# Kernel optimization log

Measured on AMD Instinct MI355X. Metric: run time of the kernel, lower is better.

The kernel has to match this reference:

```python
import jax, jax.numpy as jnp
import numpy as np

DIM = 512
NUM_HEADS = 8
HEAD_DIM = DIM // NUM_HEADS
SCALE = HEAD_DIM ** -0.5


def setup_inputs() -> dict:
    key = jax.random.key(0)
    ks = jax.random.split(key, 6)
    B, N, C = 2, 4096, DIM
    s = C ** -0.5  # init scale, torch Linear default-ish
    return {
        "x": jax.random.normal(ks[0], (B, N, C), dtype=jnp.float32),
        "Wq": jax.random.normal(ks[1], (C, C), dtype=jnp.float32) * s,
        "Wk": jax.random.normal(ks[2], (C, C), dtype=jnp.float32) * s,
        "Wv": jax.random.normal(ks[3], (C, C), dtype=jnp.float32) * s,
        "Wo": jax.random.normal(ks[4], (C, C), dtype=jnp.float32) * s,
        "bo": jax.random.normal(ks[5], (C,), dtype=jnp.float32) * s,
    }


def reference(x, Wq, Wk, Wv, Wo, bo):
    B, N, C = x.shape
    H, D = NUM_HEADS, HEAD_DIM
    # torch nn.Linear: y = x @ W.T
    q = (x @ Wq.T).reshape(B, N, H, D).transpose(0, 2, 1, 3)  # [B,H,N,D]
    k = (x @ Wk.T).reshape(B, N, H, D).transpose(0, 2, 1, 3)
    v = (x @ Wv.T).reshape(B, N, H, D).transpose(0, 2, 1, 3)
    attn = jnp.einsum("bhnd,bhmd->bhnm", q, k) * SCALE  # [B,H,N,N]
    attn = jax.nn.softmax(attn, axis=-1)
    out = jnp.einsum("bhnm,bhmd->bhnd", attn, v)
    out = out.transpose(0, 2, 1, 3).reshape(B, N, C)
    return out @ Wo.T + bo
```

## Files before the change

kernel.cpp:

```cpp
#include <hip/hip_runtime.h>
#include <hip/hip_bf16.h>
#include <cstdint>
#include <cstddef>

using bf16 = __bf16;
typedef __attribute__((ext_vector_type(8))) __bf16 bf16x8;
typedef __attribute__((ext_vector_type(4))) float  f32x4;

#define LOG2E 1.4426950408889634f

__device__ inline void gld_lds16(const void* g, void* l) {
  __builtin_amdgcn_global_load_lds(
      (const __attribute__((address_space(1))) void*)g,
      (__attribute__((address_space(3))) void*)l, 16, 0, 0);
}

__global__ __launch_bounds__(256) void k_cvt(const float* __restrict__ s,
                                             bf16* __restrict__ d, int n8) {
  int i = blockIdx.x * 256 + threadIdx.x;
  if (i >= n8) return;
  const float4* p = ((const float4*)s) + (size_t)i * 2;
  float4 a = p[0], b = p[1];
  bf16x8 o;
  o[0] = (bf16)a.x; o[1] = (bf16)a.y; o[2] = (bf16)a.z; o[3] = (bf16)a.w;
  o[4] = (bf16)b.x; o[5] = (bf16)b.y; o[6] = (bf16)b.z; o[7] = (bf16)b.w;
  *(bf16x8*)(d + (size_t)i * 8) = o;
}

__global__ __launch_bounds__(256) void k_cvtw(
    const float* __restrict__ wq, const float* __restrict__ wk,
    const float* __restrict__ wv, const float* __restrict__ wo,
    bf16* __restrict__ wqkv, bf16* __restrict__ wob) {
  int i = blockIdx.x * 256 + threadIdx.x;
  int which = i >> 15, local = i & 32767;
  const float* s = (which == 0) ? wq : (which == 1) ? wk : (which == 2) ? wv : wo;
  bf16* d = (which < 3) ? (wqkv + ((size_t)which << 18)) : wob;
  const float4* p = ((const float4*)s) + (size_t)local * 2;
  float4 a = p[0], b = p[1];
  bf16x8 o;
  o[0] = (bf16)a.x; o[1] = (bf16)a.y; o[2] = (bf16)a.z; o[3] = (bf16)a.w;
  o[4] = (bf16)b.x; o[5] = (bf16)b.y; o[6] = (bf16)b.z; o[7] = (bf16)b.w;
  *(bf16x8*)(d + (size_t)local * 8) = o;
}

__global__ __launch_bounds__(256) void k_gemm(
    const bf16* __restrict__ A, const bf16* __restrict__ B, int mode,
    bf16* __restrict__ Qb, bf16* __restrict__ Kb, bf16* __restrict__ Vtb,
    float* __restrict__ outf, const float* __restrict__ bias) {
  const int K = 512;
  __shared__ alignas(16) bf16 As[128 * 64];
  __shared__ alignas(16) bf16 Bs[64 * 64];
  const int tid = threadIdx.x;
  const int wave = tid >> 6, lane = tid & 63;
  const int l15 = lane & 15, l4 = lane >> 4;
  const int m0 = blockIdx.x * 128, n0 = blockIdx.y * 64;
  const int wr = wave >> 1, wc = wave & 1;
  f32x4 acc[4][2] = {};

  for (int k0 = 0; k0 < K; k0 += 64) {
#pragma unroll
    for (int it = 0; it < 4; ++it) {
      int c = it * 256 + tid;
      int row = c >> 3, kc = c & 7;
      int sb = (kc * 16) ^ ((row & 7) << 4);
      gld_lds16((const char*)A + ((size_t)(m0 + row) * K + k0) * 2 + sb,
                (char*)As + c * 16);
    }
#pragma unroll
    for (int it = 0; it < 2; ++it) {
      int c = it * 256 + tid;
      int row = c >> 3, kc = c & 7;
      int sb = (kc * 16) ^ ((row & 7) << 4);
      gld_lds16((const char*)B + ((size_t)(n0 + row) * K + k0) * 2 + sb,
                (char*)Bs + c * 16);
    }
    __syncthreads();
#pragma unroll
    for (int ks = 0; ks < 2; ++ks) {
      bf16x8 af[4], bff[2];
#pragma unroll
      for (int mf = 0; mf < 4; ++mf) {
        int r = wr * 64 + mf * 16 + l15;
        af[mf] = *(const bf16x8*)((const char*)As + r * 128 +
                                  ((ks * 64 + l4 * 16) ^ ((r & 7) << 4)));
      }
#pragma unroll
      for (int nf = 0; nf < 2; ++nf) {
        int r = wc * 32 + nf * 16 + l15;
        bff[nf] = *(const bf16x8*)((const char*)Bs + r * 128 +
                                   ((ks * 64 + l4 * 16) ^ ((r & 7) << 4)));
      }
#pragma unroll
      for (int mf = 0; mf < 4; ++mf)
#pragma unroll
        for (int nf = 0; nf < 2; ++nf)
          acc[mf][nf] = __builtin_amdgcn_mfma_f32_16x16x32_bf16(
              af[mf], bff[nf], acc[mf][nf], 0, 0, 0);
    }
    __syncthreads();
  }

#pragma unroll
  for (int mf = 0; mf < 4; ++mf)
#pragma unroll
    for (int nf = 0; nf < 2; ++nf)
#pragma unroll
      for (int r = 0; r < 4; ++r) {
        int m = m0 + wr * 64 + mf * 16 + l4 * 4 + r;
        int n = n0 + wc * 32 + nf * 16 + l15;
        float v = acc[mf][nf][r];
        if (mode == 1) {
          outf[(size_t)m * 512 + n] = v + bias[n];
        } else {
          int which = n >> 9, o = n & 511, h = o >> 6, d = o & 63;
          int b = m >> 12, nr = m & 4095;
          if (which == 0)
            Qb[((size_t)(b * 8 + h) * 4096 + nr) * 64 + d] = (bf16)(v * 0.125f);
          else if (which == 1)
            Kb[((size_t)(b * 8 + h) * 4096 + nr) * 64 + d] = (bf16)v;
          else
            Vtb[((size_t)((b * 8 + h) * 64 + d)) * 4096 + nr] = (bf16)v;
        }
      }
}

template <int SPLIT>
__global__ __launch_bounds__(256, 4) void k_attn_t(
    const bf16* __restrict__ Q, const bf16* __restrict__ Kg,
    const bf16* __restrict__ Vt, bf16* __restrict__ AO,
    float* __restrict__ pO, float* __restrict__ pD) {
  __shared__ alignas(16) bf16 Ks[64 * 64];
  __shared__ alignas(16) bf16 Vs[64 * 64];
  __shared__ alignas(16) bf16 Ps[4][16 * 64];
  const int tid = threadIdx.x, wave = tid >> 6, lane = tid & 63;
  const int l15 = lane & 15, l4 = lane >> 4;
  const int bh = blockIdx.y, q0 = blockIdx.x * 64;
  const int z = SPLIT ? blockIdx.z : 0;
  const int n_lo = SPLIT ? z * 2048 : 0;
  const int NT = SPLIT ? 32 : 64;
  const char* Qb = (const char*)(Q + (size_t)bh * 4096 * 64);
  const char* Kb = (const char*)(Kg + (size_t)bh * 4096 * 64);
  const char* Vb = (const char*)(Vt + (size_t)bh * 64 * 4096);

  const int c0 = tid, c1 = 256 + tid;
  const int row0 = c0 >> 3, sb0 = ((c0 & 7) * 16) ^ ((row0 & 7) << 4);
  const int row1 = c1 >> 3, sb1 = ((c1 & 7) * 16) ^ ((row1 & 7) << 4);
  const char* ksrc0 = Kb + (size_t)(n_lo + row0) * 128 + sb0;
  const char* ksrc1 = Kb + (size_t)(n_lo + row1) * 128 + sb1;
  const char* vsrc0 = Vb + (size_t)row0 * 8192 + (size_t)n_lo * 2 + sb0;
  const char* vsrc1 = Vb + (size_t)row1 * 8192 + (size_t)n_lo * 2 + sb1;
  char* kdst0 = (char*)Ks + c0 * 16;
  char* kdst1 = (char*)Ks + c1 * 16;
  char* vdst0 = (char*)Vs + c0 * 16;
  char* vdst1 = (char*)Vs + c1 * 16;

  const char* kf_p[2][4];
#pragma unroll
  for (int cf = 0; cf < 4; ++cf) {
    int kv = cf * 16 + l15;
#pragma unroll
    for (int ds = 0; ds < 2; ++ds)
      kf_p[ds][cf] = (const char*)Ks + kv * 128 +
                     ((ds * 64 + l4 * 16) ^ ((kv & 7) << 4));
  }
  const char* vf_p[4][2];
#pragma unroll
  for (int df = 0; df < 4; ++df) {
    int d = df * 16 + l15;
#pragma unroll
    for (int ks = 0; ks < 2; ++ks)
      vf_p[df][ks] = (const char*)Vs + d * 128 +
                     ((ks * 64 + l4 * 16) ^ ((d & 7) << 4));
  }
  char* pw_p[4][4];
#pragma unroll
  for (int r = 0; r < 4; ++r) {
    int q = l4 * 4 + r;
#pragma unroll
    for (int cf = 0; cf < 4; ++cf)
      pw_p[r][cf] = (char*)Ps[wave] + q * 128 +
                    (((cf * 16 + l15) * 2) ^ ((q & 7) << 4));
  }
  const char* pf_p[2];
#pragma unroll
  for (int ks = 0; ks < 2; ++ks)
    pf_p[ks] = (const char*)Ps[wave] + l15 * 128 +
               ((ks * 64 + l4 * 16) ^ ((l15 & 7) << 4));

  bf16x8 qf[2];
#pragma unroll
  for (int ds = 0; ds < 2; ++ds)
    qf[ds] = *(const bf16x8*)(Qb +
        ((size_t)(q0 + wave * 16 + l15) * 64 + ds * 32 + l4 * 8) * 2);

  bf16x8 vone;
#pragma unroll
  for (int j = 0; j < 8; ++j) vone[j] = (bf16)1.0f;

  f32x4 oacc[4] = {};
  f32x4 dacc = {};

  for (int t = 0; t < NT; ++t) {
    gld_lds16(ksrc0, kdst0);
    gld_lds16(vsrc0, vdst0);
    gld_lds16(ksrc1, kdst1);
    gld_lds16(vsrc1, vdst1);
    ksrc0 += 8192; ksrc1 += 8192;
    vsrc0 += 128;  vsrc1 += 128;
    __syncthreads();

    f32x4 s[4];
#pragma unroll
    for (int cf = 0; cf < 4; ++cf) {
      f32x4 z2 = {};
      z2 = __builtin_amdgcn_mfma_f32_16x16x32_bf16(
          qf[0], *(const bf16x8*)kf_p[0][cf], z2, 0, 0, 0);
      z2 = __builtin_amdgcn_mfma_f32_16x16x32_bf16(
          qf[1], *(const bf16x8*)kf_p[1][cf], z2, 0, 0, 0);
      s[cf] = z2;
    }

#pragma unroll
    for (int r = 0; r < 4; ++r)
#pragma unroll
      for (int cf = 0; cf < 4; ++cf) {
        float p = __builtin_amdgcn_exp2f(s[cf][r] * LOG2E);
        *(bf16*)pw_p[r][cf] = (bf16)p;
      }

    bf16x8 pf0 = *(const bf16x8*)pf_p[0];
    bf16x8 pf1 = *(const bf16x8*)pf_p[1];

    dacc = __builtin_amdgcn_mfma_f32_16x16x32_bf16(pf0, vone, dacc, 0, 0, 0);
    dacc = __builtin_amdgcn_mfma_f32_16x16x32_bf16(pf1, vone, dacc, 0, 0, 0);

#pragma unroll
    for (int df = 0; df < 4; ++df) {
      oacc[df] = __builtin_amdgcn_mfma_f32_16x16x32_bf16(
          pf0, *(const bf16x8*)vf_p[df][0], oacc[df], 0, 0, 0);
      oacc[df] = __builtin_amdgcn_mfma_f32_16x16x32_bf16(
          pf1, *(const bf16x8*)vf_p[df][1], oacc[df], 0, 0, 0);
    }
    __syncthreads();
  }

  if (SPLIT) {
    float* po = pO + (((size_t)(z * 16 + bh)) * 4096) * 64;
    float* pd = pD + ((size_t)(z * 16 + bh)) * 4096;
#pragma unroll
    for (int r = 0; r < 4; ++r) {
      int n = q0 + wave * 16 + l4 * 4 + r;
#pragma unroll
      for (int df = 0; df < 4; ++df)
        po[(size_t)n * 64 + df * 16 + l15] = oacc[df][r];
      if (l15 == 0) pd[n] = dacc[r];
    }
  } else {
    int b = bh >> 3, h = bh & 7;
#pragma unroll
    for (int r = 0; r < 4; ++r) {
      float inv = 1.0f / dacc[r];
      int n = q0 + wave * 16 + l4 * 4 + r;
#pragma unroll
      for (int df = 0; df < 4; ++df) {
        int d = df * 16 + l15;
        AO[((size_t)(b * 4096 + n)) * 512 + h * 64 + d] =
            (bf16)(oacc[df][r] * inv);
      }
    }
  }
}

__global__ __launch_bounds__(256) void k_comb(
    const float* __restrict__ pO, const float* __restrict__ pD,
    bf16* __restrict__ AO) {
  const size_t SO = (size_t)16 * 4096 * 64;
  const size_t SD = (size_t)16 * 4096;
  int i = blockIdx.x * 256 + threadIdx.x;
  int g = i >> 3, j = i & 7;
  float den = pD[g] + pD[g + SD];
  float inv = 1.0f / den;
  const float* a = pO + (size_t)g * 64 + j * 8;
  const float* b2 = a + SO;
  bf16x8 o;
#pragma unroll
  for (int t = 0; t < 8; ++t) o[t] = (bf16)((a[t] + b2[t]) * inv);
  int bh = g >> 12, n = g & 4095, b = bh >> 3, h = bh & 7;
  *(bf16x8*)(AO + ((size_t)(b * 4096 + n)) * 512 + h * 64 + j * 8) = o;
}

extern "C" void kernel_launch(void* const* d_in, const int* in_sizes, int n_in,
                              void* d_out, int out_size, void* d_ws,
                              size_t ws_size, hipStream_t stream) {
  const float* x  = (const float*)d_in[0];
  const float* Wq = (const float*)d_in[1];
  const float* Wk = (const float*)d_in[2];
  const float* Wv = (const float*)d_in[3];
  const float* Wo = (const float*)d_in[4];
  const float* bo = (const float*)d_in[5];
  float* out = (float*)d_out;

  char* ws = (char*)d_ws;
  bf16* xb   = (bf16*)(ws);
  bf16* wqkv = (bf16*)(ws + (8u << 20));
  bf16* wob  = (bf16*)(ws + (8u << 20) + 1572864u);
  bf16* Qb   = (bf16*)(ws + (10u << 20));
  bf16* Kb   = (bf16*)(ws + (18u << 20));
  bf16* Vtb  = (bf16*)(ws + (26u << 20));
  bf16* AOb  = (bf16*)(ws + (34u << 20));
  float* pD  = (float*)(ws + (42u << 20));
  float* pO  = (float*)(ws + (43u << 20));

  k_cvt<<<2048, 256, 0, stream>>>(x, xb, 524288);
  k_cvtw<<<512, 256, 0, stream>>>(Wq, Wk, Wv, Wo, wqkv, wob);

  k_gemm<<<dim3(64, 24), 256, 0, stream>>>(xb, wqkv, 0, Qb, Kb, Vtb,
                                           nullptr, nullptr);

  if (ws_size >= ((size_t)75 << 20)) {
    k_attn_t<1><<<dim3(64, 16, 2), 256, 0, stream>>>(Qb, Kb, Vtb, nullptr,
                                                     pO, pD);
    k_comb<<<2048, 256, 0, stream>>>(pO, pD, AOb);
  } else {
    k_attn_t<0><<<dim3(64, 16), 256, 0, stream>>>(Qb, Kb, Vtb, AOb,
                                                  nullptr, nullptr);
  }

  k_gemm<<<dim3(64, 8), 256, 0, stream>>>(AOb, wob, 1, nullptr, nullptr,
                                          nullptr, out, bo);
}
```

Measured before the change: 183.1 us.

## Process two 16-row query tiles per wave to reuse K/V fragments

```diff
diff --git a/kernel.cpp b/kernel.cpp
--- a/kernel.cpp
+++ b/kernel.cpp
@@ -131,10 +131,10 @@
     float* __restrict__ pO, float* __restrict__ pD) {
   __shared__ alignas(16) bf16 Ks[64 * 64];
   __shared__ alignas(16) bf16 Vs[64 * 64];
-  __shared__ alignas(16) bf16 Ps[4][16 * 64];
+  __shared__ alignas(16) bf16 Ps[4][32 * 64];
   const int tid = threadIdx.x, wave = tid >> 6, lane = tid & 63;
   const int l15 = lane & 15, l4 = lane >> 4;
-  const int bh = blockIdx.y, q0 = blockIdx.x * 64;
+  const int bh = blockIdx.y, q0 = blockIdx.x * 128;
   const int z = SPLIT ? blockIdx.z : 0;
   const int n_lo = SPLIT ? z * 2048 : 0;
   const int NT = SPLIT ? 32 : 64;
@@ -187,18 +187,20 @@
     pf_p[ks] = (const char*)Ps[wave] + l15 * 128 +
                ((ks * 64 + l4 * 16) ^ ((l15 & 7) << 4));
 
-  bf16x8 qf[2];
-#pragma unroll
-  for (int ds = 0; ds < 2; ++ds)
-    qf[ds] = *(const bf16x8*)(Qb +
-        ((size_t)(q0 + wave * 16 + l15) * 64 + ds * 32 + l4 * 8) * 2);
+  bf16x8 qf[2][2];
+#pragma unroll
+  for (int mrow = 0; mrow < 2; ++mrow)
+#pragma unroll
+    for (int ds = 0; ds < 2; ++ds)
+      qf[mrow][ds] = *(const bf16x8*)(Qb +
+          ((size_t)(q0 + wave * 32 + mrow * 16 + l15) * 64 + ds * 32 + l4 * 8) * 2);
 
   bf16x8 vone;
 #pragma unroll
   for (int j = 0; j < 8; ++j) vone[j] = (bf16)1.0f;
 
-  f32x4 oacc[4] = {};
-  f32x4 dacc = {};
+  f32x4 oacc[2][4] = {};
+  f32x4 dacc[2] = {};
 
   for (int t = 0; t < NT; ++t) {
     gld_lds16(ksrc0, kdst0);
@@ -209,37 +211,56 @@
     vsrc0 += 128;  vsrc1 += 128;
     __syncthreads();
 
-    f32x4 s[4];
+    f32x4 s[2][4];
 #pragma unroll
     for (int cf = 0; cf < 4; ++cf) {
-      f32x4 z2 = {};
-      z2 = __builtin_amdgcn_mfma_f32_16x16x32_bf16(
-          qf[0], *(const bf16x8*)kf_p[0][cf], z2, 0, 0, 0);
-      z2 = __builtin_amdgcn_mfma_f32_16x16x32_bf16(
-          qf[1], *(const bf16x8*)kf_p[1][cf], z2, 0, 0, 0);
-      s[cf] = z2;
-    }
-
-#pragma unroll
-    for (int r = 0; r < 4; ++r)
-#pragma unroll
-      for (int cf = 0; cf < 4; ++cf) {
-        float p = __builtin_amdgcn_exp2f(s[cf][r] * LOG2E);
-        *(bf16*)pw_p[r][cf] = (bf16)p;
-      }
-
-    bf16x8 pf0 = *(const bf16x8*)pf_p[0];
-    bf16x8 pf1 = *(const bf16x8*)pf_p[1];
-
-    dacc = __builtin_amdgcn_mfma_f32_16x16x32_bf16(pf0, vone, dacc, 0, 0, 0);
-    dacc = __builtin_amdgcn_mfma_f32_16x16x32_bf16(pf1, vone, dacc, 0, 0, 0);
+      bf16x8 kf0 = *(const bf16x8*)kf_p[0][cf];
+      bf16x8 kf1 = *(const bf16x8*)kf_p[1][cf];
+#pragma unroll
+      for (int mrow = 0; mrow < 2; ++mrow) {
+        f32x4 z2 = {};
+        z2 = __builtin_amdgcn_mfma_f32_16x16x32_bf16(qf[mrow][0], kf0, z2, 0, 0, 0);
+        z2 = __builtin_amdgcn_mfma_f32_16x16x32_bf16(qf[mrow][1], kf1, z2, 0, 0, 0);
+        s[mrow][cf] = z2;
+      }
+    }
+
+#pragma unroll
+    for (int mrow = 0; mrow < 2; ++mrow)
+#pragma unroll
+      for (int r = 0; r < 4; ++r)
+#pragma unroll
+        for (int cf = 0; cf < 4; ++cf) {
+          float p = __builtin_amdgcn_exp2f(s[mrow][cf][r] * LOG2E);
+          *(bf16*)(pw_p[r][cf] + mrow * 2048) = (bf16)p;
+        }
+
+    bf16x8 pf[2][2];
+#pragma unroll
+    for (int mrow = 0; mrow < 2; ++mrow) {
+      pf[mrow][0] = *(const bf16x8*)(pf_p[0] + mrow * 2048);
+      pf[mrow][1] = *(const bf16x8*)(pf_p[1] + mrow * 2048);
+    }
+
+#pragma unroll
+    for (int mrow = 0; mrow < 2; ++mrow) {
+      dacc[mrow] = __builtin_amdgcn_mfma_f32_16x16x32_bf16(pf[mrow][0], vone,
+                                                           dacc[mrow], 0, 0, 0);
+      dacc[mrow] = __builtin_amdgcn_mfma_f32_16x16x32_bf16(pf[mrow][1], vone,
+                                                           dacc[mrow], 0, 0, 0);
+    }
 
 #pragma unroll
     for (int df = 0; df < 4; ++df) {
-      oacc[df] = __builtin_amdgcn_mfma_f32_16x16x32_bf16(
-          pf0, *(const bf16x8*)vf_p[df][0], oacc[df], 0, 0, 0);
-      oacc[df] = __builtin_amdgcn_mfma_f32_16x16x32_bf16(
-          pf1, *(const bf16x8*)vf_p[df][1], oacc[df], 0, 0, 0);
+      bf16x8 vf0 = *(const bf16x8*)vf_p[df][0];
+      bf16x8 vf1 = *(const bf16x8*)vf_p[df][1];
+#pragma unroll
+      for (int mrow = 0; mrow < 2; ++mrow) {
+        oacc[mrow][df] = __builtin_amdgcn_mfma_f32_16x16x32_bf16(
+            pf[mrow][0], vf0, oacc[mrow][df], 0, 0, 0);
+        oacc[mrow][df] = __builtin_amdgcn_mfma_f32_16x16x32_bf16(
+            pf[mrow][1], vf1, oacc[mrow][df], 0, 0, 0);
+      }
     }
     __syncthreads();
   }
@@ -248,26 +269,30 @@
     float* po = pO + (((size_t)(z * 16 + bh)) * 4096) * 64;
     float* pd = pD + ((size_t)(z * 16 + bh)) * 4096;
 #pragma unroll
-    for (int r = 0; r < 4; ++r) {
-      int n = q0 + wave * 16 + l4 * 4 + r;
-#pragma unroll
-      for (int df = 0; df < 4; ++df)
-        po[(size_t)n * 64 + df * 16 + l15] = oacc[df][r];
-      if (l15 == 0) pd[n] = dacc[r];
-    }
+    for (int mrow = 0; mrow < 2; ++mrow)
+#pragma unroll
+      for (int r = 0; r < 4; ++r) {
+        int n = q0 + wave * 32 + mrow * 16 + l4 * 4 + r;
+#pragma unroll
+        for (int df = 0; df < 4; ++df)
+          po[(size_t)n * 64 + df * 16 + l15] = oacc[mrow][df][r];
+        if (l15 == 0) pd[n] = dacc[mrow][r];
+      }
   } else {
     int b = bh >> 3, h = bh & 7;
 #pragma unroll
-    for (int r = 0; r < 4; ++r) {
-      float inv = 1.0f / dacc[r];
-      int n = q0 + wave * 16 + l4 * 4 + r;
-#pragma unroll
-      for (int df = 0; df < 4; ++df) {
-        int d = df * 16 + l15;
-        AO[((size_t)(b * 4096 + n)) * 512 + h * 64 + d] =
-            (bf16)(oacc[df][r] * inv);
-      }
-    }
+    for (int mrow = 0; mrow < 2; ++mrow)
+#pragma unroll
+      for (int r = 0; r < 4; ++r) {
+        float inv = 1.0f / dacc[mrow][r];
+        int n = q0 + wave * 32 + mrow * 16 + l4 * 4 + r;
+#pragma unroll
+        for (int df = 0; df < 4; ++df) {
+          int d = df * 16 + l15;
+          AO[((size_t)(b * 4096 + n)) * 512 + h * 64 + d] =
+              (bf16)(oacc[mrow][df][r] * inv);
+        }
+      }
   }
 }
 
@@ -318,11 +343,11 @@
                                            nullptr, nullptr);
 
   if (ws_size >= ((size_t)75 << 20)) {
-    k_attn_t<1><<<dim3(64, 16, 2), 256, 0, stream>>>(Qb, Kb, Vtb, nullptr,
+    k_attn_t<1><<<dim3(32, 16, 2), 256, 0, stream>>>(Qb, Kb, Vtb, nullptr,
                                                      pO, pD);
     k_comb<<<2048, 256, 0, stream>>>(pO, pD, AOb);
   } else {
-    k_attn_t<0><<<dim3(64, 16), 256, 0, stream>>>(Qb, Kb, Vtb, AOb,
+    k_attn_t<0><<<dim3(32, 16), 256, 0, stream>>>(Qb, Kb, Vtb, AOb,
                                                   nullptr, nullptr);
   }
 
```

Measured after the change: 160.9 us. 12.1% less time.
